# Kernel tuning notes

Measured on AMD Instinct MI355X. Metric: run time of the kernel, lower is better.

Reference implementation:

```python
import jax, jax.numpy as jnp
import numpy as np

HIDDEN = 2048
NUM_HEADS = 16
HEAD_DIM = HIDDEN // NUM_HEADS
WORLD_SIZE = 4
BATCH = 1
SEQ_SHARD = 2048


def setup_inputs() -> dict:
    key = jax.random.key(0)
    ks = jax.random.split(key, 9)
    s = 1.0 / np.sqrt(HIDDEN)
    return {
        'hidden_states': jax.random.normal(ks[0], (BATCH, SEQ_SHARD, HIDDEN), jnp.float32),
        'wq': jax.random.normal(ks[1], (HIDDEN, HIDDEN), jnp.float32) * s,
        'bq': jax.random.normal(ks[2], (HIDDEN,), jnp.float32) * s,
        'wk': jax.random.normal(ks[3], (HIDDEN, HIDDEN), jnp.float32) * s,
        'bk': jax.random.normal(ks[4], (HIDDEN,), jnp.float32) * s,
        'wv': jax.random.normal(ks[5], (HIDDEN, HIDDEN), jnp.float32) * s,
        'bv': jax.random.normal(ks[6], (HIDDEN,), jnp.float32) * s,
        'wo': jax.random.normal(ks[7], (HIDDEN, HIDDEN), jnp.float32) * s,
        'bo': jax.random.normal(ks[8], (HIDDEN,), jnp.float32) * s,
    }


def _ring_attention(q, k, v):
    # q, k, v: [B, H, S, D]. Simulation: every ring step receives the SAME
    # local KV shard (all_k_shards are clones of k), accumulated with
    # flash-style online softmax across WORLD_SIZE steps.
    B, H, S, D = q.shape
    scale = 1.0 / np.sqrt(D)
    output_acc = jnp.zeros_like(q)
    max_score = jnp.full((B, H, S, 1), -jnp.inf, dtype=q.dtype)
    sum_exp = jnp.zeros((B, H, S, 1), dtype=q.dtype)
    for _ in range(WORLD_SIZE):  # fixed small loop over ring steps
        scores = jnp.einsum('bhsd,bhtd->bhst', q, k) * scale  # [B,H,S,S]
        new_max = jnp.max(scores, axis=-1, keepdims=True)
        combined_max = jnp.maximum(max_score, new_max)
        old_scale = jnp.exp(max_score - combined_max)
        new_scale = jnp.exp(new_max - combined_max)
        new_exp = jnp.exp(scores - new_max)
        sum_exp = sum_exp * old_scale + jnp.sum(new_exp, axis=-1, keepdims=True) * new_scale
        output_acc = output_acc * old_scale + jnp.einsum('bhst,bhtd->bhsd', new_exp, v) * new_scale
        max_score = combined_max
    return output_acc / sum_exp


def reference(hidden_states, wq, bq, wk, bk, wv, bv, wo, bo):
    B, S, _ = hidden_states.shape
    # nn.Linear: y = x @ W^T + b
    q = hidden_states @ wq.T + bq
    k = hidden_states @ wk.T + bk
    v = hidden_states @ wv.T + bv
    split = lambda t: t.reshape(B, S, NUM_HEADS, HEAD_DIM).transpose(0, 2, 1, 3)
    attn = _ring_attention(split(q), split(k), split(v))  # [B,H,S,D]
    attn = attn.transpose(0, 2, 1, 3).reshape(B, S, HIDDEN)
    return attn @ wo.T + bo
```

## Files before the change

kernel.cpp:

```cpp
#include <hip/hip_runtime.h>
#include <hip/hip_bf16.h>
#include <stdint.h>

#define SEQ 2048
#define HID 2048
#define NH 16
#define HD 128
#define QSCALE_L2E 0.1275304429019769f

typedef __attribute__((ext_vector_type(4))) float f32x4;
typedef __attribute__((ext_vector_type(8))) short short8;
typedef __attribute__((ext_vector_type(4))) float f4;
typedef __attribute__((ext_vector_type(4))) unsigned short us4;

__device__ __forceinline__ unsigned short f2bu(float f) {
  union { float f; unsigned int u; } c; c.f = f;
  unsigned int u = c.u + 0x7fffu + ((c.u >> 16) & 1u);
  return (unsigned short)(u >> 16);
}

__device__ __forceinline__ unsigned short f2bu_fast(float f) {
  union { float f; unsigned int u; } c; c.f = f;
  return (unsigned short)((c.u + 0x8000u) >> 16);
}

__device__ __forceinline__ float b2f(unsigned short u) {
  union { unsigned int u; float f; } c; c.u = ((unsigned int)u) << 16; return c.f;
}

__device__ __forceinline__ float exp2fast(float x) {
  float r; asm("v_exp_f32 %0, %1" : "=v"(r) : "v"(x)); return r;
}

__device__ __forceinline__ void gload_lds16(const void* g, void* l) {
  __builtin_amdgcn_global_load_lds((const __attribute__((address_space(1))) void*)g,
                                   (__attribute__((address_space(3))) void*)l, 16, 0, 0);
}

#define BAR() __builtin_amdgcn_s_barrier()
#define LGKM0() do { asm volatile("s_waitcnt lgkmcnt(0)" ::: "memory"); __builtin_amdgcn_sched_barrier(0); } while (0)
#define VM6()   do { asm volatile("s_waitcnt vmcnt(6)"   ::: "memory"); __builtin_amdgcn_sched_barrier(0); } while (0)
#define VM0()   do { asm volatile("s_waitcnt vmcnt(0)"   ::: "memory"); __builtin_amdgcn_sched_barrier(0); } while (0)

__global__ __launch_bounds__(256) void cvt_kernel(
    const float* __restrict__ s0, const float* __restrict__ s1,
    const float* __restrict__ s2, const float* __restrict__ s3,
    const float* __restrict__ s4,
    unsigned short* __restrict__ d0, unsigned short* __restrict__ d1,
    unsigned short* __restrict__ d2, unsigned short* __restrict__ d3,
    unsigned short* __restrict__ d4, int n)
{
  const float* s; unsigned short* d;
  switch (blockIdx.y) {
    case 0: s = s0; d = d0; break;
    case 1: s = s1; d = d1; break;
    case 2: s = s2; d = d2; break;
    case 3: s = s3; d = d3; break;
    default: s = s4; d = d4; break;
  }
  const int stride = gridDim.x * blockDim.x;
  for (int i = blockIdx.x * blockDim.x + threadIdx.x; i * 8 < n; i += stride) {
    f4 v0 = *(const f4*)&s[i * 8];
    f4 v1 = *(const f4*)&s[i * 8 + 4];
    short8 o;
    o[0] = (short)f2bu(v0[0]); o[1] = (short)f2bu(v0[1]);
    o[2] = (short)f2bu(v0[2]); o[3] = (short)f2bu(v0[3]);
    o[4] = (short)f2bu(v1[0]); o[5] = (short)f2bu(v1[1]);
    o[6] = (short)f2bu(v1[2]); o[7] = (short)f2bu(v1[3]);
    *(short8*)&d[i * 8] = o;
  }
}

template<int MODE>
__global__ __launch_bounds__(256, 2) void gemm128(
    const unsigned short* __restrict__ A,
    const unsigned short* __restrict__ B,
    const float* __restrict__ b0, const float* __restrict__ b1, const float* __restrict__ b2,
    unsigned short* __restrict__ O0, unsigned short* __restrict__ O1, unsigned short* __restrict__ O2,
    float* __restrict__ Of, int M, int N, int K)
{
  constexpr int ASZ = 64 * 64;
  constexpr int BSZ = 128 * 64;

  extern __shared__ unsigned short lds[];
  const int tid = threadIdx.x;
  const int lane = tid & 63, w = tid >> 6;
  const int g = lane >> 4, q = lane & 15;
  const long bm = (long)blockIdx.y * 64, bn = (long)blockIdx.x * 128;
  const int NK = K >> 6;

  const int srl = lane >> 3;
  const int scE = ((lane & 7) ^ srl) * 8;
  const int c0 = (g ^ (q & 7)) * 8;
  const int c1 = c0 ^ 32;
  const int aB = q * 64;
  const int bB = (w * 32 + q) * 64;

  f32x4 acc[4][2] = {};
  short8 a[4][2], b[2][2];

#define STAGE_A(jj) do {                                                      \
    unsigned short* dst_ = lds + (((jj) & 1) ? ASZ : 0);                      \
    _Pragma("unroll")                                                         \
    for (int c_ = 0; c_ < 2; ++c_) {                                          \
      const long row_ = (c_ * 4 + w) * 8 + srl;                               \
      gload_lds16(&A[(bm + row_) * (long)K + (jj) * 64 + scE],                \
                  &dst_[(c_ * 4 + w) * 512]);                                 \
    }                                                                         \
  } while (0)

#define STAGE_B(jj) do {                                                      \
    unsigned short* dst_ = lds + 2 * ASZ + (((jj) & 1) ? BSZ : 0);            \
    _Pragma("unroll")                                                         \
    for (int c_ = 0; c_ < 4; ++c_) {                                          \
      const long row_ = (c_ * 4 + w) * 8 + srl;                               \
      gload_lds16(&B[(bn + row_) * (long)K + (jj) * 64 + scE],                \
                  &dst_[(c_ * 4 + w) * 512]);                                 \
    }                                                                         \
  } while (0)

#define QUAD8(ni)                                                             \
  do {                                                                        \
    __builtin_amdgcn_s_setprio(1);                                            \
    _Pragma("unroll")                                                         \
    for (int mi_ = 0; mi_ < 4; ++mi_) {                                       \
      acc[mi_][ni] = __builtin_amdgcn_mfma_f32_16x16x32_bf16(                 \
          a[mi_][0], b[ni][0], acc[mi_][ni], 0, 0, 0);                        \
      acc[mi_][ni] = __builtin_amdgcn_mfma_f32_16x16x32_bf16(                 \
          a[mi_][1], b[ni][1], acc[mi_][ni], 0, 0, 0);                        \
    }                                                                         \
    __builtin_amdgcn_s_setprio(0);                                            \
  } while (0)

  STAGE_A(0); STAGE_B(0);
  STAGE_A(1); STAGE_B(1);
  VM6();
  BAR();

  for (int j = 0; j < NK; ++j) {
    unsigned short* At = lds + ((j & 1) ? ASZ : 0);
    unsigned short* Bt = lds + 2 * ASZ + ((j & 1) ? BSZ : 0);

#pragma unroll
    for (int mi = 0; mi < 4; ++mi) {
      a[mi][0] = *(const short8*)&At[aB + mi * 1024 + c0];
      a[mi][1] = *(const short8*)&At[aB + mi * 1024 + c1];
    }
#pragma unroll
    for (int ni = 0; ni < 2; ++ni) {
      b[ni][0] = *(const short8*)&Bt[bB + ni * 1024 + c0];
      b[ni][1] = *(const short8*)&Bt[bB + ni * 1024 + c1];
    }
    QUAD8(0);
    LGKM0();
    BAR();
    if (j + 2 < NK) { STAGE_A(j + 2); STAGE_B(j + 2); }
    QUAD8(1);
    if (j < NK - 2) { VM6(); } else { VM0(); }
    BAR();
  }

#pragma unroll
  for (int ni = 0; ni < 2; ++ni) {
    const int col = (int)bn + w * 32 + ni * 16 + q;
    float bv;
    if (MODE == 4) {
      const int which = col >> 11, c = col & 2047;
      const float* bp = which == 0 ? b0 : (which == 1 ? b1 : b2);
      bv = bp[c];
    } else {
      bv = b0[col];
    }
#pragma unroll
    for (int mi = 0; mi < 4; ++mi)
#pragma unroll
      for (int r = 0; r < 4; ++r) {
        const long row = bm + mi * 16 + 4 * g + r;
        const float v = acc[mi][ni][r] + bv;
        if (MODE == 4) {
          const int which = col >> 11, c = col & 2047, head = c >> 7, d = c & 127;
          if (which == 0)      O0[((long)head * SEQ + row) * HD + d] = f2bu(v * QSCALE_L2E);
          else if (which == 1) O1[((long)head * SEQ + row) * HD + d] = f2bu(v);
          else                 O2[((long)head * HD + d) * SEQ + row] = f2bu(v);
        } else {
          Of[row * (long)N + col] = v;
        }
      }
  }
#undef STAGE_A
#undef STAGE_B
#undef QUAD8
}

#define KVB 64
__global__ __launch_bounds__(256) void flash_attn(
    const unsigned short* __restrict__ Qb,
    const unsigned short* __restrict__ Kb,
    const unsigned short* __restrict__ VTb,
    unsigned short* __restrict__ Po,
    float* __restrict__ Pl)
{
  __shared__ __align__(16) unsigned short Kt[64 * 128];
  __shared__ __align__(16) unsigned short Vt[128 * 64];
  __shared__ __align__(16) unsigned short Pt[4][16 * 64];
  const int tid = threadIdx.x;
  const int l = tid & 63, w = tid >> 6;
  const int g = l >> 4, q = l & 15;
  const int h = blockIdx.y, qb = blockIdx.x, half = blockIdx.z;
  const int qrow0 = qb * 64 + w * 16;

  short8 qf[4];
#pragma unroll
  for (int dc = 0; dc < 4; ++dc)
    qf[dc] = *(const short8*)&Qb[((long)h * SEQ + qrow0 + q) * HD + dc * 32 + g * 8];

  f32x4 oacc[8] = {};
  float lsum[4] = {0.f, 0.f, 0.f, 0.f};

  const int kr = tid >> 4, kc16 = tid & 15;
  const int vr = tid >> 3, vc8 = tid & 7;
  const unsigned short* Kg = Kb + (long)h * SEQ * HD + (long)half * 1024 * HD;
  const unsigned short* Vg = VTb + (long)h * HD * SEQ + half * 1024;

  short8 kreg[4], vreg[4];
#pragma unroll
  for (int it = 0; it < 4; ++it) {
    kreg[it] = *(const short8*)&Kg[(long)(kr + it * 16) * HD + kc16 * 8];
    vreg[it] = *(const short8*)&Vg[(long)(vr + it * 32) * SEQ + vc8 * 8];
  }

  for (int kb = 0; kb < 1024; kb += KVB) {
    __syncthreads();
#pragma unroll
    for (int it = 0; it < 4; ++it) {
      const int krow = kr + it * 16;
      *(short8*)&Kt[((krow * 256 + kc16 * 16) ^ ((krow & 7) << 4)) >> 1] = kreg[it];
      const int vrow = vr + it * 32;
      *(short8*)&Vt[((vrow * 128 + vc8 * 16) ^ ((vrow & 7) << 4)) >> 1] = vreg[it];
    }
    __syncthreads();
    if (kb + KVB < 1024) {
#pragma unroll
      for (int it = 0; it < 4; ++it) {
        kreg[it] = *(const short8*)&Kg[(long)(kb + KVB + kr + it * 16) * HD + kc16 * 8];
        vreg[it] = *(const short8*)&Vg[(long)(vr + it * 32) * SEQ + kb + KVB + vc8 * 8];
      }
    }

    f32x4 sacc[4] = {};
#pragma unroll
    for (int kc = 0; kc < 4; ++kc) {
      const int krow = kc * 16 + q;
      const int sw = (krow & 7) << 4;
#pragma unroll
      for (int dc = 0; dc < 4; ++dc) {
        short8 kf = *(const short8*)&Kt[((krow * 256 + dc * 64 + g * 16) ^ sw) >> 1];
        sacc[kc] = __builtin_amdgcn_mfma_f32_16x16x32_bf16(qf[dc], kf, sacc[kc], 0, 0, 0);
      }
    }

    float p[4][4];
#pragma unroll
    for (int r = 0; r < 4; ++r) {
#pragma unroll
      for (int kc = 0; kc < 4; ++kc) p[kc][r] = exp2fast(sacc[kc][r]);
      lsum[r] += (p[0][r] + p[1][r]) + (p[2][r] + p[3][r]);
    }

    unsigned short* Pw = &Pt[w][0];
#pragma unroll
    for (int r = 0; r < 4; ++r) {
      const int prow = 4 * g + r;
      const int sw = (prow & 7) << 4;
#pragma unroll
      for (int kc = 0; kc < 4; ++kc)
        Pw[((prow * 128 + (kc * 16 + q) * 2) ^ sw) >> 1] = f2bu_fast(p[kc][r]);
    }

    short8 pf[2];
    const int psw = (q & 7) << 4;
#pragma unroll
    for (int ks = 0; ks < 2; ++ks)
      pf[ks] = *(const short8*)&Pw[((q * 128 + ks * 64 + g * 16) ^ psw) >> 1];
#pragma unroll
    for (int dt = 0; dt < 8; ++dt) {
      const int vrow = dt * 16 + q;
#pragma unroll
      for (int ks = 0; ks < 2; ++ks) {
        short8 vf = *(const short8*)&Vt[((vrow * 128 + ks * 64 + g * 16) ^ psw) >> 1];
        oacc[dt] = __builtin_amdgcn_mfma_f32_16x16x32_bf16(pf[ks], vf, oacc[dt], 0, 0, 0);
      }
    }
  }

#pragma unroll
  for (int off = 1; off < 16; off <<= 1)
#pragma unroll
    for (int r = 0; r < 4; ++r) lsum[r] += __shfl_xor(lsum[r], off);

  const long tI = ((long)h * 32 + qb) * 2 + half;
  unsigned short* PoT = Po + tI * 8192;
#pragma unroll
  for (int dt = 0; dt < 8; ++dt)
#pragma unroll
    for (int r = 0; r < 4; ++r)
      PoT[(w * 16 + 4 * g + r) * 128 + dt * 16 + q] = f2bu_fast(oacc[dt][r]);
  if (q == 0) {
#pragma unroll
    for (int r = 0; r < 4; ++r)
      Pl[tI * 64 + w * 16 + 4 * g + r] = lsum[r];
  }
}

__global__ __launch_bounds__(256) void combine_kernel(
    const unsigned short* __restrict__ Po, const float* __restrict__ Pl,
    unsigned short* __restrict__ attnb)
{
  const int qb = blockIdx.x, h = blockIdx.y;
  const long tI = ((long)h * 32 + qb) * 2;
  const unsigned short* A0 = Po + tI * 8192;
  const unsigned short* A1 = Po + (tI + 1) * 8192;
  const float* L0 = Pl + tI * 64;
  const float* L1 = Pl + (tI + 1) * 64;
  const int tid = threadIdx.x;
#pragma unroll
  for (int k = 0; k < 8; ++k) {
    const int i = tid + k * 256;
    const int row = i >> 5, c4 = i & 31;
    const us4 a = *(const us4*)&A0[i * 4];
    const us4 b = *(const us4*)&A1[i * 4];
    const float rl = 1.f / (L0[row] + L1[row]);
    us4 o;
    o[0] = f2bu((b2f(a[0]) + b2f(b[0])) * rl);
    o[1] = f2bu((b2f(a[1]) + b2f(b[1])) * rl);
    o[2] = f2bu((b2f(a[2]) + b2f(b[2])) * rl);
    o[3] = f2bu((b2f(a[3]) + b2f(b[3])) * rl);
    *(us4*)&attnb[(long)(qb * 64 + row) * HID + h * HD + c4 * 4] = o;
  }
}

extern "C" void kernel_launch(void* const* d_in, const int* in_sizes, int n_in,
                              void* d_out, int out_size, void* d_ws, size_t ws_size,
                              hipStream_t stream)
{
  const float* x  = (const float*)d_in[0];
  const float* wq = (const float*)d_in[1];
  const float* bq = (const float*)d_in[2];
  const float* wk = (const float*)d_in[3];
  const float* bk = (const float*)d_in[4];
  const float* wv = (const float*)d_in[5];
  const float* bv = (const float*)d_in[6];
  const float* wo = (const float*)d_in[7];
  const float* bo = (const float*)d_in[8];

  const long NEL = (long)HID * HID;
  unsigned short* Xb   = (unsigned short*)d_ws;
  unsigned short* Wqkv = Xb + NEL;
  unsigned short* Wob  = Wqkv + 3 * NEL;
  unsigned short* Qbuf = Wob + NEL;
  unsigned short* Kbuf = Qbuf + NEL;
  unsigned short* VTb  = Kbuf + NEL;
  unsigned short* Attn = VTb + NEL;

  unsigned short* Po = (unsigned short*)d_ws;
  float* Pl = (float*)d_out;

  cvt_kernel<<<dim3(512, 5), 256, 0, stream>>>(
      x, wq, wk, wv, wo, Xb, Wqkv, Wqkv + NEL, Wqkv + 2 * NEL, Wob, (int)NEL);

  gemm128<4><<<dim3(48, 32), 256, 49152, stream>>>(
      Xb, Wqkv, bq, bk, bv, Qbuf, Kbuf, VTb, nullptr, SEQ, 3 * HID, HID);

  flash_attn<<<dim3(SEQ / 64, NH, 2), 256, 0, stream>>>(Qbuf, Kbuf, VTb, Po, Pl);

  combine_kernel<<<dim3(SEQ / 64, NH), 256, 0, stream>>>(Po, Pl, Attn);

  gemm128<3><<<dim3(16, 32), 256, 49152, stream>>>(
      Attn, Wob, bo, nullptr, nullptr, nullptr, nullptr, nullptr,
      (float*)d_out, SEQ, HID, HID);
}
```

Measured before the change: 182.5 us.

## Add 256x256-tile 8-wave GEMM with double-buffered LDS for QKV projection

Introduces a new gemm256 kernel with 256x256 output tiles, 512 threads (8 waves) and a 128 KB double-buffered LDS pipeline that interleaves global-to-LDS staging with MFMA phases, using s_setprio around the MFMA bursts. The fused QKV projection is switched from gemm128 (64x128 tiles, 1536 blocks) to this kernel (192 blocks). Larger tiles raise arithmetic intensity and operand reuse. The cost is only 192 workgroups on a 256-CU device, which leaves some CUs idle, and one-time setup of the dynamic LDS attribute.

```diff
diff --git a/kernel.cpp b/kernel.cpp
--- a/kernel.cpp
+++ b/kernel.cpp
@@ -69,6 +69,152 @@
     o[6] = (short)f2bu(v1[2]); o[7] = (short)f2bu(v1[3]);
     *(short8*)&d[i * 8] = o;
   }
+}
+
+template<int MODE>
+__global__ __launch_bounds__(512, 2) void gemm256(
+    const unsigned short* __restrict__ A,
+    const unsigned short* __restrict__ B,
+    const float* __restrict__ b0, const float* __restrict__ b1, const float* __restrict__ b2,
+    unsigned short* __restrict__ O0, unsigned short* __restrict__ O1, unsigned short* __restrict__ O2,
+    float* __restrict__ Of, int M, int N, int K)
+{
+  extern __shared__ unsigned short lds[];
+  const int tid = threadIdx.x;
+  const int l = tid & 63, w = tid >> 6;
+  const int g = l >> 4, q = l & 15;
+  const int wgM = w >> 2, wgN = w & 3;
+  const long bm = (long)blockIdx.y * 256, bn = (long)blockIdx.x * 256;
+  const int NK = K >> 6;
+
+  const int srl = l >> 3;
+  const int scE = ((l & 7) ^ srl) * 8;
+  const unsigned short* aG = A + (bm + w * 8 + srl) * (long)K + scE;
+  const unsigned short* bG = B + (bn + w * 8 + srl) * (long)K + scE;
+  const int stReg = w * 512;
+
+  const int cA0 = (g ^ (q & 7)) * 8;
+  const int rowA = (wgM * 64 + q) * 64;
+  const int rowB = (wgN * 32 + q) * 64;
+
+  f32x4 acc[8][4] = {};
+  short8 a[4][2], bb[4][2];
+
+#define STG(gp, halfRow, jj, ldsEl)                                           \
+  do {                                                                        \
+    _Pragma("unroll")                                                         \
+    for (int c_ = 0; c_ < 2; ++c_)                                            \
+      gload_lds16((gp) + ((long)((halfRow) + c_ * 64)) * K + (jj) * 64,       \
+                  &lds[(ldsEl) + c_ * 4096 + stReg]);                         \
+  } while (0)
+
+#define LDA(h, be)                                                            \
+  do { const unsigned short* At_ = &lds[(be) + (h) * 8192 + rowA];            \
+    _Pragma("unroll")                                                         \
+    for (int mi_ = 0; mi_ < 4; ++mi_) {                                       \
+      a[mi_][0] = *(const short8*)&At_[mi_ * 1024 + cA0];                     \
+      a[mi_][1] = *(const short8*)&At_[mi_ * 1024 + (cA0 ^ 32)];              \
+    } } while (0)
+
+#define LDB(h, be)                                                            \
+  do { const unsigned short* Bt_ = &lds[(be) + 16384 + (h) * 8192 + rowB];    \
+    _Pragma("unroll")                                                         \
+    for (int ni_ = 0; ni_ < 2; ++ni_) {                                       \
+      bb[(h) * 2 + ni_][0] = *(const short8*)&Bt_[ni_ * 1024 + cA0];          \
+      bb[(h) * 2 + ni_][1] = *(const short8*)&Bt_[ni_ * 1024 + (cA0 ^ 32)];   \
+    } } while (0)
+
+#define MF16(mb, nA, nB)                                                      \
+  do { __builtin_amdgcn_s_setprio(1);                                         \
+    _Pragma("unroll")                                                         \
+    for (int mi_ = 0; mi_ < 4; ++mi_) {                                       \
+      acc[(mb) + mi_][nA] = __builtin_amdgcn_mfma_f32_16x16x32_bf16(          \
+          a[mi_][0], bb[nA][0], acc[(mb) + mi_][nA], 0, 0, 0);                \
+      acc[(mb) + mi_][nA] = __builtin_amdgcn_mfma_f32_16x16x32_bf16(          \
+          a[mi_][1], bb[nA][1], acc[(mb) + mi_][nA], 0, 0, 0);                \
+      acc[(mb) + mi_][nB] = __builtin_amdgcn_mfma_f32_16x16x32_bf16(          \
+          a[mi_][0], bb[nB][0], acc[(mb) + mi_][nB], 0, 0, 0);                \
+      acc[(mb) + mi_][nB] = __builtin_amdgcn_mfma_f32_16x16x32_bf16(          \
+          a[mi_][1], bb[nB][1], acc[(mb) + mi_][nB], 0, 0, 0);                \
+    }                                                                         \
+    __builtin_amdgcn_s_setprio(0); } while (0)
+
+  STG(aG, 0,   0, 0);
+  STG(aG, 128, 0, 8192);
+  STG(bG, 0,   0, 16384);
+  STG(bG, 128, 0, 24576);
+  if (NK > 1) {
+    STG(aG, 0,   1, 32768);
+    STG(bG, 0,   1, 32768 + 16384);
+    STG(bG, 128, 1, 32768 + 24576);
+    VM6();
+  } else {
+    VM0();
+  }
+  BAR();
+
+  for (int j = 0; j < NK; ++j) {
+    const int b0e = (j & 1) << 15;
+    const int b1e = b0e ^ 32768;
+
+    LDA(0, b0e); LDB(0, b0e);
+    if (j + 1 < NK) STG(aG, 128, j + 1, b1e + 8192);
+    BAR(); LGKM0();
+    MF16(0, 0, 1);
+    BAR();
+
+    LDB(1, b0e);
+    if (j + 2 < NK) STG(aG, 0, j + 2, b0e);
+    BAR(); LGKM0();
+    MF16(0, 2, 3);
+    BAR();
+
+    LDA(1, b0e);
+    if (j + 2 < NK) STG(bG, 0, j + 2, b0e + 16384);
+    BAR(); LGKM0();
+    MF16(4, 0, 1);
+    BAR();
+
+    if (j + 2 < NK) STG(bG, 128, j + 2, b0e + 24576);
+    BAR();
+    MF16(4, 2, 3);
+    if (j + 2 < NK) { VM6(); } else { VM0(); }
+    BAR();
+  }
+
+#pragma unroll
+  for (int ni = 0; ni < 4; ++ni) {
+    const int col = (int)bn + (ni >> 1) * 128 + wgN * 32 + (ni & 1) * 16 + q;
+    float bv;
+    if (MODE == 4) {
+      const int which = col >> 11, c = col & 2047;
+      const float* bp = which == 0 ? b0 : (which == 1 ? b1 : b2);
+      bv = bp[c];
+    } else {
+      bv = b0[col];
+    }
+#pragma unroll
+    for (int mi = 0; mi < 8; ++mi) {
+      const long row0 = bm + (mi >> 2) * 128 + wgM * 64 + (mi & 3) * 16 + 4 * g;
+#pragma unroll
+      for (int r = 0; r < 4; ++r) {
+        const long row = row0 + r;
+        const float v = acc[mi][ni][r] + bv;
+        if (MODE == 4) {
+          const int which = col >> 11, c = col & 2047, head = c >> 7, d = c & 127;
+          if (which == 0)      O0[((long)head * SEQ + row) * HD + d] = f2bu(v * QSCALE_L2E);
+          else if (which == 1) O1[((long)head * SEQ + row) * HD + d] = f2bu(v);
+          else                 O2[((long)head * HD + d) * SEQ + row] = f2bu(v);
+        } else {
+          Of[row * (long)N + col] = v;
+        }
+      }
+    }
+  }
+#undef STG
+#undef LDA
+#undef LDB
+#undef MF16
 }
 
 template<int MODE>
@@ -365,10 +511,17 @@
   unsigned short* Po = (unsigned short*)d_ws;
   float* Pl = (float*)d_out;
 
+  static bool attrDone = false;
+  if (!attrDone) {
+    hipFuncSetAttribute(reinterpret_cast<const void*>(gemm256<4>),
+                        hipFuncAttributeMaxDynamicSharedMemorySize, 131072);
+    attrDone = true;
+  }
+
   cvt_kernel<<<dim3(512, 5), 256, 0, stream>>>(
       x, wq, wk, wv, wo, Xb, Wqkv, Wqkv + NEL, Wqkv + 2 * NEL, Wob, (int)NEL);
 
-  gemm128<4><<<dim3(48, 32), 256, 49152, stream>>>(
+  gemm256<4><<<dim3(24, 8), 512, 131072, stream>>>(
       Xb, Wqkv, bq, bk, bv, Qbuf, Kbuf, VTb, nullptr, SEQ, 3 * HID, HID);
 
   flash_attn<<<dim3(SEQ / 64, NH, 2), 256, 0, stream>>>(Qbuf, Kbuf, VTb, Po, Pl);
```

Measured after the change: 192.9 us. 1.06x slower.

## Enlarge GEMM tiles to 128x128 with 2x2 warp layout

Applied to the files above, without the earlier changes.

Both the QKV and output-projection GEMMs move from 64x128 tiles to 128x128 tiles, with each of the four waves computing a 64x64 sub-tile in a 2x2 arrangement. This doubles the MFMA work per LDS load and cuts global reloads of the A and B operands. The cost is more accumulator registers, 64KB of LDS per block set through a function attribute, and half as many blocks. The smaller grid (256 blocks for the output GEMM) may underfill the GPU's CUs.

```diff
diff --git a/kernel.cpp b/kernel.cpp
--- a/kernel.cpp
+++ b/kernel.cpp
@@ -39,7 +39,7 @@
 
 #define BAR() __builtin_amdgcn_s_barrier()
 #define LGKM0() do { asm volatile("s_waitcnt lgkmcnt(0)" ::: "memory"); __builtin_amdgcn_sched_barrier(0); } while (0)
-#define VM6()   do { asm volatile("s_waitcnt vmcnt(6)"   ::: "memory"); __builtin_amdgcn_sched_barrier(0); } while (0)
+#define VM8()   do { asm volatile("s_waitcnt vmcnt(8)"   ::: "memory"); __builtin_amdgcn_sched_barrier(0); } while (0)
 #define VM0()   do { asm volatile("s_waitcnt vmcnt(0)"   ::: "memory"); __builtin_amdgcn_sched_barrier(0); } while (0)
 
 __global__ __launch_bounds__(256) void cvt_kernel(
@@ -72,74 +72,68 @@
 }
 
 template<int MODE>
-__global__ __launch_bounds__(256, 2) void gemm128(
+__global__ __launch_bounds__(256, 2) void gemm128sq(
     const unsigned short* __restrict__ A,
     const unsigned short* __restrict__ B,
     const float* __restrict__ b0, const float* __restrict__ b1, const float* __restrict__ b2,
     unsigned short* __restrict__ O0, unsigned short* __restrict__ O1, unsigned short* __restrict__ O2,
     float* __restrict__ Of, int M, int N, int K)
 {
-  constexpr int ASZ = 64 * 64;
-  constexpr int BSZ = 128 * 64;
+  constexpr int TSZ = 128 * 64;
 
   extern __shared__ unsigned short lds[];
   const int tid = threadIdx.x;
   const int lane = tid & 63, w = tid >> 6;
   const int g = lane >> 4, q = lane & 15;
-  const long bm = (long)blockIdx.y * 64, bn = (long)blockIdx.x * 128;
+  const int wgM = w >> 1, wgN = w & 1;
+  const long bm = (long)blockIdx.y * 128, bn = (long)blockIdx.x * 128;
   const int NK = K >> 6;
 
   const int srl = lane >> 3;
   const int scE = ((lane & 7) ^ srl) * 8;
   const int c0 = (g ^ (q & 7)) * 8;
   const int c1 = c0 ^ 32;
-  const int aB = q * 64;
-  const int bB = (w * 32 + q) * 64;
-
-  f32x4 acc[4][2] = {};
-  short8 a[4][2], b[2][2];
-
-#define STAGE_A(jj) do {                                                      \
-    unsigned short* dst_ = lds + (((jj) & 1) ? ASZ : 0);                      \
+  const int aB = (wgM * 64 + q) * 64;
+  const int bB = (wgN * 64 + q) * 64;
+
+  f32x4 acc[4][4] = {};
+  short8 a[4][2], b[4][2];
+
+#define STAGE(gp, gbase, jj, ldsOff) do {                                     \
+    unsigned short* dst_ = lds + (ldsOff) + (((jj) & 1) ? TSZ : 0);           \
     _Pragma("unroll")                                                         \
-    for (int c_ = 0; c_ < 2; ++c_) {                                          \
+    for (int c_ = 0; c_ < 4; ++c_) {                                          \
       const long row_ = (c_ * 4 + w) * 8 + srl;                               \
-      gload_lds16(&A[(bm + row_) * (long)K + (jj) * 64 + scE],                \
+      gload_lds16(&(gp)[((gbase) + row_) * (long)K + (jj) * 64 + scE],        \
                   &dst_[(c_ * 4 + w) * 512]);                                 \
     }                                                                         \
   } while (0)
 
-#define STAGE_B(jj) do {                                                      \
-    unsigned short* dst_ = lds + 2 * ASZ + (((jj) & 1) ? BSZ : 0);            \
-    _Pragma("unroll")                                                         \
-    for (int c_ = 0; c_ < 4; ++c_) {                                          \
-      const long row_ = (c_ * 4 + w) * 8 + srl;                               \
-      gload_lds16(&B[(bn + row_) * (long)K + (jj) * 64 + scE],                \
-                  &dst_[(c_ * 4 + w) * 512]);                                 \
-    }                                                                         \
-  } while (0)
-
-#define QUAD8(ni)                                                             \
+#define QUADD(n0, n1)                                                         \
   do {                                                                        \
     __builtin_amdgcn_s_setprio(1);                                            \
     _Pragma("unroll")                                                         \
     for (int mi_ = 0; mi_ < 4; ++mi_) {                                       \
-      acc[mi_][ni] = __builtin_amdgcn_mfma_f32_16x16x32_bf16(                 \
-          a[mi_][0], b[ni][0], acc[mi_][ni], 0, 0, 0);                        \
-      acc[mi_][ni] = __builtin_amdgcn_mfma_f32_16x16x32_bf16(                 \
-          a[mi_][1], b[ni][1], acc[mi_][ni], 0, 0, 0);                        \
+      acc[mi_][n0] = __builtin_amdgcn_mfma_f32_16x16x32_bf16(                 \
+          a[mi_][0], b[n0][0], acc[mi_][n0], 0, 0, 0);                        \
+      acc[mi_][n0] = __builtin_amdgcn_mfma_f32_16x16x32_bf16(                 \
+          a[mi_][1], b[n0][1], acc[mi_][n0], 0, 0, 0);                        \
+      acc[mi_][n1] = __builtin_amdgcn_mfma_f32_16x16x32_bf16(                 \
+          a[mi_][0], b[n1][0], acc[mi_][n1], 0, 0, 0);                        \
+      acc[mi_][n1] = __builtin_amdgcn_mfma_f32_16x16x32_bf16(                 \
+          a[mi_][1], b[n1][1], acc[mi_][n1], 0, 0, 0);                        \
     }                                                                         \
     __builtin_amdgcn_s_setprio(0);                                            \
   } while (0)
 
-  STAGE_A(0); STAGE_B(0);
-  STAGE_A(1); STAGE_B(1);
-  VM6();
+  STAGE(A, bm, 0, 0); STAGE(B, bn, 0, 2 * TSZ);
+  STAGE(A, bm, 1, 0); STAGE(B, bn, 1, 2 * TSZ);
+  VM8();
   BAR();
 
   for (int j = 0; j < NK; ++j) {
-    unsigned short* At = lds + ((j & 1) ? ASZ : 0);
-    unsigned short* Bt = lds + 2 * ASZ + ((j & 1) ? BSZ : 0);
+    const unsigned short* At = lds + ((j & 1) ? TSZ : 0);
+    const unsigned short* Bt = lds + 2 * TSZ + ((j & 1) ? TSZ : 0);
 
 #pragma unroll
     for (int mi = 0; mi < 4; ++mi) {
@@ -147,22 +141,22 @@
       a[mi][1] = *(const short8*)&At[aB + mi * 1024 + c1];
     }
 #pragma unroll
-    for (int ni = 0; ni < 2; ++ni) {
+    for (int ni = 0; ni < 4; ++ni) {
       b[ni][0] = *(const short8*)&Bt[bB + ni * 1024 + c0];
       b[ni][1] = *(const short8*)&Bt[bB + ni * 1024 + c1];
     }
-    QUAD8(0);
+    QUADD(0, 1);
     LGKM0();
     BAR();
-    if (j + 2 < NK) { STAGE_A(j + 2); STAGE_B(j + 2); }
-    QUAD8(1);
-    if (j < NK - 2) { VM6(); } else { VM0(); }
+    if (j + 2 < NK) { STAGE(A, bm, j + 2, 0); STAGE(B, bn, j + 2, 2 * TSZ); }
+    QUADD(2, 3);
+    if (j < NK - 2) { VM8(); } else { VM0(); }
     BAR();
   }
 
 #pragma unroll
-  for (int ni = 0; ni < 2; ++ni) {
-    const int col = (int)bn + w * 32 + ni * 16 + q;
+  for (int ni = 0; ni < 4; ++ni) {
+    const int col = (int)bn + wgN * 64 + ni * 16 + q;
     float bv;
     if (MODE == 4) {
       const int which = col >> 11, c = col & 2047;
@@ -175,7 +169,7 @@
     for (int mi = 0; mi < 4; ++mi)
 #pragma unroll
       for (int r = 0; r < 4; ++r) {
-        const long row = bm + mi * 16 + 4 * g + r;
+        const long row = bm + wgM * 64 + mi * 16 + 4 * g + r;
         const float v = acc[mi][ni][r] + bv;
         if (MODE == 4) {
           const int which = col >> 11, c = col & 2047, head = c >> 7, d = c & 127;
@@ -187,9 +181,8 @@
         }
       }
   }
-#undef STAGE_A
-#undef STAGE_B
-#undef QUAD8
+#undef STAGE
+#undef QUADD
 }
 
 #define KVB 64
@@ -365,17 +358,26 @@
   unsigned short* Po = (unsigned short*)d_ws;
   float* Pl = (float*)d_out;
 
+  static bool attrDone = false;
+  if (!attrDone) {
+    hipFuncSetAttribute(reinterpret_cast<const void*>(gemm128sq<4>),
+                        hipFuncAttributeMaxDynamicSharedMemorySize, 65536);
+    hipFuncSetAttribute(reinterpret_cast<const void*>(gemm128sq<3>),
+                        hipFuncAttributeMaxDynamicSharedMemorySize, 65536);
+    attrDone = true;
+  }
+
   cvt_kernel<<<dim3(512, 5), 256, 0, stream>>>(
       x, wq, wk, wv, wo, Xb, Wqkv, Wqkv + NEL, Wqkv + 2 * NEL, Wob, (int)NEL);
 
-  gemm128<4><<<dim3(48, 32), 256, 49152, stream>>>(
+  gemm128sq<4><<<dim3(48, 16), 256, 65536, stream>>>(
       Xb, Wqkv, bq, bk, bv, Qbuf, Kbuf, VTb, nullptr, SEQ, 3 * HID, HID);
 
   flash_attn<<<dim3(SEQ / 64, NH, 2), 256, 0, stream>>>(Qbuf, Kbuf, VTb, Po, Pl);
 
   combine_kernel<<<dim3(SEQ / 64, NH), 256, 0, stream>>>(Po, Pl, Attn);
 
-  gemm128<3><<<dim3(16, 32), 256, 49152, stream>>>(
+  gemm128sq<3><<<dim3(16, 16), 256, 65536, stream>>>(
       Attn, Wob, bo, nullptr, nullptr, nullptr, nullptr, nullptr,
       (float*)d_out, SEQ, HID, HID);
 }
```

Result: no change. 185.5 us (+1.6%).

## Drop split-KV in flash attention and fuse normalization into epilogue

Applied to the files above, without the earlier changes.

Removes the two-way split over the key/value sequence and the separate combine kernel; each attention block now walks all 2048 keys and writes the normalized bf16 output straight into the attention buffer. This saves one kernel launch and the round trip of partial outputs and row sums through memory. In exchange the grid halves to 512 blocks, which lowers parallelism across the compute units, and each block does twice as many sequential KV iterations.

```diff
diff --git a/kernel.cpp b/kernel.cpp
--- a/kernel.cpp
+++ b/kernel.cpp
@@ -197,8 +197,7 @@
     const unsigned short* __restrict__ Qb,
     const unsigned short* __restrict__ Kb,
     const unsigned short* __restrict__ VTb,
-    unsigned short* __restrict__ Po,
-    float* __restrict__ Pl)
+    unsigned short* __restrict__ attnb)
 {
   __shared__ __align__(16) unsigned short Kt[64 * 128];
   __shared__ __align__(16) unsigned short Vt[128 * 64];
@@ -206,7 +205,7 @@
   const int tid = threadIdx.x;
   const int l = tid & 63, w = tid >> 6;
   const int g = l >> 4, q = l & 15;
-  const int h = blockIdx.y, qb = blockIdx.x, half = blockIdx.z;
+  const int h = blockIdx.y, qb = blockIdx.x;
   const int qrow0 = qb * 64 + w * 16;
 
   short8 qf[4];
@@ -219,8 +218,8 @@
 
   const int kr = tid >> 4, kc16 = tid & 15;
   const int vr = tid >> 3, vc8 = tid & 7;
-  const unsigned short* Kg = Kb + (long)h * SEQ * HD + (long)half * 1024 * HD;
-  const unsigned short* Vg = VTb + (long)h * HD * SEQ + half * 1024;
+  const unsigned short* Kg = Kb + (long)h * SEQ * HD;
+  const unsigned short* Vg = VTb + (long)h * HD * SEQ;
 
   short8 kreg[4], vreg[4];
 #pragma unroll
@@ -229,7 +228,7 @@
     vreg[it] = *(const short8*)&Vg[(long)(vr + it * 32) * SEQ + vc8 * 8];
   }
 
-  for (int kb = 0; kb < 1024; kb += KVB) {
+  for (int kb = 0; kb < SEQ; kb += KVB) {
     __syncthreads();
 #pragma unroll
     for (int it = 0; it < 4; ++it) {
@@ -239,7 +238,7 @@
       *(short8*)&Vt[((vrow * 128 + vc8 * 16) ^ ((vrow & 7) << 4)) >> 1] = vreg[it];
     }
     __syncthreads();
-    if (kb + KVB < 1024) {
+    if (kb + KVB < SEQ) {
 #pragma unroll
       for (int it = 0; it < 4; ++it) {
         kreg[it] = *(const short8*)&Kg[(long)(kb + KVB + kr + it * 16) * HD + kc16 * 8];
@@ -298,44 +297,15 @@
 #pragma unroll
     for (int r = 0; r < 4; ++r) lsum[r] += __shfl_xor(lsum[r], off);
 
-  const long tI = ((long)h * 32 + qb) * 2 + half;
-  unsigned short* PoT = Po + tI * 8192;
-#pragma unroll
-  for (int dt = 0; dt < 8; ++dt)
-#pragma unroll
-    for (int r = 0; r < 4; ++r)
-      PoT[(w * 16 + 4 * g + r) * 128 + dt * 16 + q] = f2bu_fast(oacc[dt][r]);
-  if (q == 0) {
-#pragma unroll
-    for (int r = 0; r < 4; ++r)
-      Pl[tI * 64 + w * 16 + 4 * g + r] = lsum[r];
-  }
-}
-
-__global__ __launch_bounds__(256) void combine_kernel(
-    const unsigned short* __restrict__ Po, const float* __restrict__ Pl,
-    unsigned short* __restrict__ attnb)
-{
-  const int qb = blockIdx.x, h = blockIdx.y;
-  const long tI = ((long)h * 32 + qb) * 2;
-  const unsigned short* A0 = Po + tI * 8192;
-  const unsigned short* A1 = Po + (tI + 1) * 8192;
-  const float* L0 = Pl + tI * 64;
-  const float* L1 = Pl + (tI + 1) * 64;
-  const int tid = threadIdx.x;
-#pragma unroll
-  for (int k = 0; k < 8; ++k) {
-    const int i = tid + k * 256;
-    const int row = i >> 5, c4 = i & 31;
-    const us4 a = *(const us4*)&A0[i * 4];
-    const us4 b = *(const us4*)&A1[i * 4];
-    const float rl = 1.f / (L0[row] + L1[row]);
-    us4 o;
-    o[0] = f2bu((b2f(a[0]) + b2f(b[0])) * rl);
-    o[1] = f2bu((b2f(a[1]) + b2f(b[1])) * rl);
-    o[2] = f2bu((b2f(a[2]) + b2f(b[2])) * rl);
-    o[3] = f2bu((b2f(a[3]) + b2f(b[3])) * rl);
-    *(us4*)&attnb[(long)(qb * 64 + row) * HID + h * HD + c4 * 4] = o;
+  const float rl0 = 1.f / lsum[0], rl1 = 1.f / lsum[1];
+  const float rl2 = 1.f / lsum[2], rl3 = 1.f / lsum[3];
+#pragma unroll
+  for (int dt = 0; dt < 8; ++dt) {
+    const long colb = (long)h * HD + dt * 16 + q;
+    attnb[(long)(qrow0 + 4 * g + 0) * HID + colb] = f2bu(oacc[dt][0] * rl0);
+    attnb[(long)(qrow0 + 4 * g + 1) * HID + colb] = f2bu(oacc[dt][1] * rl1);
+    attnb[(long)(qrow0 + 4 * g + 2) * HID + colb] = f2bu(oacc[dt][2] * rl2);
+    attnb[(long)(qrow0 + 4 * g + 3) * HID + colb] = f2bu(oacc[dt][3] * rl3);
   }
 }
 
@@ -362,18 +332,13 @@
   unsigned short* VTb  = Kbuf + NEL;
   unsigned short* Attn = VTb + NEL;
 
-  unsigned short* Po = (unsigned short*)d_ws;
-  float* Pl = (float*)d_out;
-
   cvt_kernel<<<dim3(512, 5), 256, 0, stream>>>(
       x, wq, wk, wv, wo, Xb, Wqkv, Wqkv + NEL, Wqkv + 2 * NEL, Wob, (int)NEL);
 
   gemm128<4><<<dim3(48, 32), 256, 49152, stream>>>(
       Xb, Wqkv, bq, bk, bv, Qbuf, Kbuf, VTb, nullptr, SEQ, 3 * HID, HID);
 
-  flash_attn<<<dim3(SEQ / 64, NH, 2), 256, 0, stream>>>(Qbuf, Kbuf, VTb, Po, Pl);
-
-  combine_kernel<<<dim3(SEQ / 64, NH), 256, 0, stream>>>(Po, Pl, Attn);
+  flash_attn<<<dim3(SEQ / 64, NH), 256, 0, stream>>>(Qbuf, Kbuf, VTb, Attn);
 
   gemm128<3><<<dim3(16, 32), 256, 49152, stream>>>(
       Attn, Wob, bo, nullptr, nullptr, nullptr, nullptr, nullptr,
```

Result: faster. 176.4 us (-3.3%).
